# Performance work log

Hardware: AMD Instinct MI355X
Metric: run time of the kernel (lower is better)

The kernel has to match this reference:

```python
import jax, jax.numpy as jnp
import numpy as np

N = 100000
E = 6400000
DIMS = [34, 16, 16, 16, 4]


def setup_inputs() -> dict:
    key = jax.random.key(0)
    ks = jax.random.split(key, 12)
    x = jax.random.normal(ks[0], (N, DIMS[0]), dtype=jnp.float32)
    edge_index = jax.random.randint(ks[1], (2, E), 0, N, dtype=jnp.int64)
    inp = {"x": x, "edge_index": edge_index}
    for i in range(4):
        fan_in, fan_out = DIMS[i], DIMS[i + 1]
        s = (6.0 / (fan_in + fan_out)) ** 0.5  # glorot
        inp[f"W{i+1}"] = jax.random.uniform(ks[2 + 2 * i], (fan_in, fan_out), minval=-s, maxval=s, dtype=jnp.float32)
        inp[f"b{i+1}"] = jnp.zeros((fan_out,), dtype=jnp.float32)
    return inp


def gcn_layer(x, W, b, src, dst, norm):
    # x: [N, din] -> [N, dout]; PyG GCNConv: h = XW, aggregate norm*h[src] into dst, + bias
    h = x @ W
    msgs = h[src] * norm[:, None]                      # [E+N, dout]
    out = jax.ops.segment_sum(msgs, dst, num_segments=N)
    return out + b


def reference(x, edge_index, W1, b1, W2, b2, W3, b3, W4, b4):
    loop = jnp.arange(N, dtype=edge_index.dtype)
    src = jnp.concatenate([edge_index[0], loop])       # add self-loops
    dst = jnp.concatenate([edge_index[1], loop])
    deg = jax.ops.segment_sum(jnp.ones_like(dst, dtype=x.dtype), dst, num_segments=N)
    dinv = jnp.where(deg > 0, jax.lax.rsqrt(deg), 0.0)
    norm = dinv[src] * dinv[dst]                       # symmetric normalization per edge
    h = gcn_layer(x, W1, b1, src, dst, norm)
    h = jax.nn.relu(h)
    h = gcn_layer(h, W2, b2, src, dst, norm)
    h = jax.nn.relu(h)
    h = gcn_layer(h, W3, b3, src, dst, norm)
    h = jax.nn.relu(h)
    return gcn_layer(h, W4, b4, src, dst, norm)
```

## Files before the change

kernel.cpp:

```cpp
#include <hip/hip_runtime.h>
#include <hip/hip_bf16.h>


static constexpr int THREADS   = 256;
static constexpr int BSHIFT    = 7;
static constexpr int NPB       = 128;
static constexpr int MAXB      = 1024;
static constexpr int NCHUNK    = 128;
static constexpr int EPT       = 8;
static constexpr int SSHIFT    = 15;
static constexpr int NSHARD    = 4;
static constexpr int STAGE_CAP = 10240;


__global__ __launch_bounds__(THREADS)
void k_hist(const int* __restrict__ dst, int* __restrict__ hist_part,
            int e, int nbkt, int chunk) {
    __shared__ int h[MAXB];
    for (int t = threadIdx.x; t < nbkt; t += THREADS) h[t] = 0;
    __syncthreads();
    int beg = blockIdx.x * chunk;
    int end = min(e, beg + chunk);
    for (int base = beg; base < end; base += THREADS * EPT) {
        int i = base + (int)threadIdx.x * EPT;
        if (i + EPT <= end) {
            int4 d0 = *(const int4*)(dst + i);
            int4 d1 = *(const int4*)(dst + i + 4);
            atomicAdd(&h[d0.x >> BSHIFT], 1);
            atomicAdd(&h[d0.y >> BSHIFT], 1);
            atomicAdd(&h[d0.z >> BSHIFT], 1);
            atomicAdd(&h[d0.w >> BSHIFT], 1);
            atomicAdd(&h[d1.x >> BSHIFT], 1);
            atomicAdd(&h[d1.y >> BSHIFT], 1);
            atomicAdd(&h[d1.z >> BSHIFT], 1);
            atomicAdd(&h[d1.w >> BSHIFT], 1);
        } else {
            for (int k = i; k < end; k++) atomicAdd(&h[dst[k] >> BSHIFT], 1);
        }
    }
    __syncthreads();
    for (int t = threadIdx.x; t < nbkt; t += THREADS)
        hist_part[(size_t)blockIdx.x * nbkt + t] = h[t];
}

__global__ __launch_bounds__(NCHUNK)
void k_colscan(int* __restrict__ hist_part, int* __restrict__ btot, int nbkt) {
    __shared__ int s[NCHUNK];
    int b = blockIdx.x;
    int v = hist_part[(size_t)threadIdx.x * nbkt + b];
    s[threadIdx.x] = v;
    __syncthreads();
    for (int ofs = 1; ofs < NCHUNK; ofs <<= 1) {
        int t = (threadIdx.x >= ofs) ? s[threadIdx.x - ofs] : 0;
        __syncthreads();
        s[threadIdx.x] += t;
        __syncthreads();
    }
    hist_part[(size_t)threadIdx.x * nbkt + b] = s[threadIdx.x] - v;
    if (threadIdx.x == NCHUNK - 1) btot[b] = s[NCHUNK - 1];
}

__global__ __launch_bounds__(1024)
void k_scan_b(const int* __restrict__ btot, int* __restrict__ bbase,
              int nbkt, int e) {
    __shared__ int s[1024];
    int v = (threadIdx.x < nbkt) ? btot[threadIdx.x] : 0;
    s[threadIdx.x] = v;
    __syncthreads();
    for (int ofs = 1; ofs < 1024; ofs <<= 1) {
        int t = (threadIdx.x >= ofs) ? s[threadIdx.x - ofs] : 0;
        __syncthreads();
        s[threadIdx.x] += t;
        __syncthreads();
    }
    if (threadIdx.x < nbkt) bbase[threadIdx.x] = s[threadIdx.x] - v;
    if (threadIdx.x == 0) bbase[nbkt] = e;
}

__global__ __launch_bounds__(THREADS)
void k_scatter_bkt(const int* __restrict__ src, const int* __restrict__ dst,
                   const int* __restrict__ offs_part, const int* __restrict__ bbase,
                   int* __restrict__ gpack, int e, int nbkt, int chunk) {
    __shared__ int curs[MAXB];
    for (int t = threadIdx.x; t < nbkt; t += THREADS)
        curs[t] = bbase[t] + offs_part[(size_t)blockIdx.x * nbkt + t];
    __syncthreads();
    int beg = blockIdx.x * chunk;
    int end = min(e, beg + chunk);
    for (int base = beg; base < end; base += THREADS * EPT) {
        int i = base + (int)threadIdx.x * EPT;
        if (i + EPT <= end) {
            int4 s0 = *(const int4*)(src + i);
            int4 s1 = *(const int4*)(src + i + 4);
            int4 d0 = *(const int4*)(dst + i);
            int4 d1 = *(const int4*)(dst + i + 4);
            int p0 = atomicAdd(&curs[d0.x >> BSHIFT], 1);
            int p1 = atomicAdd(&curs[d0.y >> BSHIFT], 1);
            int p2 = atomicAdd(&curs[d0.z >> BSHIFT], 1);
            int p3 = atomicAdd(&curs[d0.w >> BSHIFT], 1);
            int p4 = atomicAdd(&curs[d1.x >> BSHIFT], 1);
            int p5 = atomicAdd(&curs[d1.y >> BSHIFT], 1);
            int p6 = atomicAdd(&curs[d1.z >> BSHIFT], 1);
            int p7 = atomicAdd(&curs[d1.w >> BSHIFT], 1);
            gpack[p0] = (s0.x << BSHIFT) | (d0.x & (NPB - 1));
            gpack[p1] = (s0.y << BSHIFT) | (d0.y & (NPB - 1));
            gpack[p2] = (s0.z << BSHIFT) | (d0.z & (NPB - 1));
            gpack[p3] = (s0.w << BSHIFT) | (d0.w & (NPB - 1));
            gpack[p4] = (s1.x << BSHIFT) | (d1.x & (NPB - 1));
            gpack[p5] = (s1.y << BSHIFT) | (d1.y & (NPB - 1));
            gpack[p6] = (s1.z << BSHIFT) | (d1.z & (NPB - 1));
            gpack[p7] = (s1.w << BSHIFT) | (d1.w & (NPB - 1));
        } else {
            for (int k = i; k < end; k++) {
                int d = dst[k];
                int p = atomicAdd(&curs[d >> BSHIFT], 1);
                gpack[p] = (src[k] << BSHIFT) | (d & (NPB - 1));
            }
        }
    }
}

__global__ __launch_bounds__(THREADS)
void k_rowptr2(const int* __restrict__ gpack, const int* __restrict__ bbase,
               int* __restrict__ rowptr2, float* __restrict__ dinv,
               int n, int nbkt) {
    __shared__ int hist2[NPB * NSHARD];
    __shared__ int scn[THREADS];
    int b = blockIdx.x;
    int node0 = b << BSHIFT;
    int nnodes = min(NPB, n - node0);
    int ebeg = bbase[b];
    int eend = bbase[b + 1];
    int tid = threadIdx.x;

    for (int t = tid; t < NPB * NSHARD; t += THREADS) hist2[t] = 0;
    __syncthreads();
    for (int i = ebeg + tid; i < eend; i += THREADS) {
        int g = gpack[i];
        int key = (g & (NPB - 1)) * NSHARD + ((g >> BSHIFT) >> SSHIFT);
        atomicAdd(&hist2[key], 1);
    }
    __syncthreads();
    int v0 = 0, v1 = 0, v2 = 0, v3 = 0, tsum = 0;
    if (tid < NPB) {
        v0 = hist2[tid * NSHARD + 0];
        v1 = hist2[tid * NSHARD + 1];
        v2 = hist2[tid * NSHARD + 2];
        v3 = hist2[tid * NSHARD + 3];
        tsum = v0 + v1 + v2 + v3;
    }
    scn[tid] = tsum;
    __syncthreads();
    for (int ofs = 1; ofs < THREADS; ofs <<= 1) {
        int t = (tid >= ofs) ? scn[tid - ofs] : 0;
        __syncthreads();
        scn[tid] += t;
        __syncthreads();
    }
    int excl = scn[tid] - tsum;
    if (tid < nnodes) {
        int nd = node0 + tid;
        rowptr2[(size_t)nd * NSHARD + 0] = ebeg + excl;
        rowptr2[(size_t)nd * NSHARD + 1] = ebeg + excl + v0;
        rowptr2[(size_t)nd * NSHARD + 2] = ebeg + excl + v0 + v1;
        rowptr2[(size_t)nd * NSHARD + 3] = ebeg + excl + v0 + v1 + v2;
        dinv[nd] = 1.0f / sqrtf((float)(tsum + 1));
    }
    if (b == nbkt - 1 && tid == 0) rowptr2[(size_t)n * NSHARD] = eend;
}

__global__ __launch_bounds__(THREADS)
void k_fill_staged(const int* __restrict__ gpack, const int* __restrict__ bbase,
                   const int* __restrict__ rowptr2, int* __restrict__ csr,
                   int n, int nbkt) {
    __shared__ int curs[NPB * NSHARD];
    __shared__ int staged[STAGE_CAP];
    int b = blockIdx.x;
    int node0 = b << BSHIFT;
    int tid = threadIdx.x;
    int ebeg = bbase[b];
    int eend = bbase[b + 1];
    int len = eend - ebeg;

    for (int t = tid; t < NPB * NSHARD; t += THREADS) {
        int nd = node0 + (t >> 2);
        curs[t] = (nd < n) ? rowptr2[(size_t)nd * NSHARD + (t & 3)] : 0;
    }
    __syncthreads();

    if (len <= STAGE_CAP) {
        for (int i = ebeg + tid; i < eend; i += THREADS) {
            int g = gpack[i];
            int key = (g & (NPB - 1)) * NSHARD + ((g >> BSHIFT) >> SSHIFT);
            int pos = atomicAdd(&curs[key], 1);
            staged[pos - ebeg] = g >> BSHIFT;
        }
        __syncthreads();
        for (int i = tid; i < len; i += THREADS)
            csr[ebeg + i] = staged[i];
    } else {
        for (int i = ebeg + tid; i < eend; i += THREADS) {
            int g = gpack[i];
            int key = (g & (NPB - 1)) * NSHARD + ((g >> BSHIFT) >> SSHIFT);
            int pos = atomicAdd(&curs[key], 1);
            csr[pos] = g >> BSHIFT;
        }
    }
}


__global__ __launch_bounds__(THREADS)
void k_layer_in(const float* __restrict__ x, const float* __restrict__ W,
                const float* __restrict__ dinv, float* __restrict__ hp, int n) {
    __shared__ float sW[34 * 16];
    for (int t = threadIdx.x; t < 34 * 16; t += THREADS) sW[t] = W[t];
    __syncthreads();
    int i = blockIdx.x * THREADS + threadIdx.x;
    if (i >= n) return;
    float di = dinv[i];
    float acc[16];
    #pragma unroll
    for (int j = 0; j < 16; j++) acc[j] = 0.0f;
    const float* xi = x + (size_t)i * 34;
    #pragma unroll
    for (int k = 0; k < 34; k++) {
        float xk = xi[k];
        #pragma unroll
        for (int j = 0; j < 16; j++) acc[j] = fmaf(xk, sW[k * 16 + j], acc[j]);
    }
    float4* o = (float4*)(hp + (size_t)i * 16);
    o[0] = make_float4(acc[0] * di, acc[1] * di, acc[2] * di, acc[3] * di);
    o[1] = make_float4(acc[4] * di, acc[5] * di, acc[6] * di, acc[7] * di);
    o[2] = make_float4(acc[8] * di, acc[9] * di, acc[10] * di, acc[11] * di);
    o[3] = make_float4(acc[12] * di, acc[13] * di, acc[14] * di, acc[15] * di);
}

__global__ __launch_bounds__(THREADS)
void k_layer_mid2(const float* __restrict__ part, const float* __restrict__ W,
                  const float* __restrict__ bprev, const float* __restrict__ dinv,
                  float* __restrict__ hp, int n) {
    __shared__ float sW[16 * 16];
    __shared__ float sB[16];
    for (int t = threadIdx.x; t < 16 * 16; t += THREADS) sW[t] = W[t];
    if (threadIdx.x < 16) sB[threadIdx.x] = bprev[threadIdx.x];
    __syncthreads();
    int i = blockIdx.x * THREADS + threadIdx.x;
    if (i >= n) return;
    float di = dinv[i];
    size_t stride = (size_t)n * 4;
    const float4* p = (const float4*)(part + (size_t)i * 16);
    float4 a0 = p[0], a1 = p[1], a2 = p[2], a3 = p[3];
    #pragma unroll
    for (int s = 1; s < NSHARD; s++) {
        float4 q0 = p[s * stride + 0], q1 = p[s * stride + 1];
        float4 q2 = p[s * stride + 2], q3 = p[s * stride + 3];
        a0.x += q0.x; a0.y += q0.y; a0.z += q0.z; a0.w += q0.w;
        a1.x += q1.x; a1.y += q1.y; a1.z += q1.z; a1.w += q1.w;
        a2.x += q2.x; a2.y += q2.y; a2.z += q2.z; a2.w += q2.w;
        a3.x += q3.x; a3.y += q3.y; a3.z += q3.z; a3.w += q3.w;
    }
    float xin[16] = {a0.x, a0.y, a0.z, a0.w, a1.x, a1.y, a1.z, a1.w,
                     a2.x, a2.y, a2.z, a2.w, a3.x, a3.y, a3.z, a3.w};
    #pragma unroll
    for (int k = 0; k < 16; k++)
        xin[k] = fmaxf(fmaf(di, xin[k], sB[k]), 0.0f);
    float acc[16];
    #pragma unroll
    for (int j = 0; j < 16; j++) acc[j] = 0.0f;
    #pragma unroll
    for (int k = 0; k < 16; k++) {
        float xk = xin[k];
        #pragma unroll
        for (int j = 0; j < 16; j++) acc[j] = fmaf(xk, sW[k * 16 + j], acc[j]);
    }
    float4* o = (float4*)(hp + (size_t)i * 16);
    o[0] = make_float4(acc[0] * di, acc[1] * di, acc[2] * di, acc[3] * di);
    o[1] = make_float4(acc[4] * di, acc[5] * di, acc[6] * di, acc[7] * di);
    o[2] = make_float4(acc[8] * di, acc[9] * di, acc[10] * di, acc[11] * di);
    o[3] = make_float4(acc[12] * di, acc[13] * di, acc[14] * di, acc[15] * di);
}

__global__ __launch_bounds__(THREADS)
void k_layer_last2(const float* __restrict__ part, const float* __restrict__ W,
                   const float* __restrict__ bprev, const float* __restrict__ dinv,
                   float* __restrict__ hp4, int n) {
    __shared__ float sW[16 * 4];
    __shared__ float sB[16];
    for (int t = threadIdx.x; t < 16 * 4; t += THREADS) sW[t] = W[t];
    if (threadIdx.x < 16) sB[threadIdx.x] = bprev[threadIdx.x];
    __syncthreads();
    int i = blockIdx.x * THREADS + threadIdx.x;
    if (i >= n) return;
    float di = dinv[i];
    size_t stride = (size_t)n * 4;
    const float4* p = (const float4*)(part + (size_t)i * 16);
    float4 a0 = p[0], a1 = p[1], a2 = p[2], a3 = p[3];
    #pragma unroll
    for (int s = 1; s < NSHARD; s++) {
        float4 q0 = p[s * stride + 0], q1 = p[s * stride + 1];
        float4 q2 = p[s * stride + 2], q3 = p[s * stride + 3];
        a0.x += q0.x; a0.y += q0.y; a0.z += q0.z; a0.w += q0.w;
        a1.x += q1.x; a1.y += q1.y; a1.z += q1.z; a1.w += q1.w;
        a2.x += q2.x; a2.y += q2.y; a2.z += q2.z; a2.w += q2.w;
        a3.x += q3.x; a3.y += q3.y; a3.z += q3.z; a3.w += q3.w;
    }
    float xin[16] = {a0.x, a0.y, a0.z, a0.w, a1.x, a1.y, a1.z, a1.w,
                     a2.x, a2.y, a2.z, a2.w, a3.x, a3.y, a3.z, a3.w};
    #pragma unroll
    for (int k = 0; k < 16; k++)
        xin[k] = fmaxf(fmaf(di, xin[k], sB[k]), 0.0f);
    float acc[4];
    #pragma unroll
    for (int j = 0; j < 4; j++) acc[j] = 0.0f;
    #pragma unroll
    for (int k = 0; k < 16; k++) {
        float xk = xin[k];
        #pragma unroll
        for (int j = 0; j < 4; j++) acc[j] = fmaf(xk, sW[k * 4 + j], acc[j]);
    }
    *(float4*)(hp4 + (size_t)i * 4) =
        make_float4(acc[0] * di, acc[1] * di, acc[2] * di, acc[3] * di);
}


__global__ __launch_bounds__(THREADS, 8)
void k_gather16s(const int* __restrict__ rowptr2, const int* __restrict__ csr,
                 const float* __restrict__ hp, float* __restrict__ part, int n) {
    int shard = blockIdx.x & (NSHARD - 1);
    int rg    = blockIdx.x >> 2;
    int row   = rg * 16 + ((int)threadIdx.x >> 4);
    int lane  = threadIdx.x & 15;
    if (row >= n) return;
    int base = (threadIdx.x & 63) & ~15;

    int beg = rowptr2[(size_t)row * NSHARD + shard];
    int end = rowptr2[(size_t)row * NSHARD + shard + 1];
    int len = end - beg;

    float a0 = ((row >> SSHIFT) == shard) ? hp[(size_t)row * 16 + lane] : 0.0f;
    float a1 = 0.f, a2 = 0.f, a3 = 0.f;

    int s0 = 0, s1 = 0;
    if (len > 0)  s0 = csr[min(beg + lane, end - 1)];
    if (len > 16) s1 = csr[min(beg + 16 + lane, end - 1)];

    {
        int cnt = len;
        #pragma unroll
        for (int k = 0; k < 16; k += 4) {
            int sk0 = __shfl(s0, base + k + 0, 64);
            int sk1 = __shfl(s0, base + k + 1, 64);
            int sk2 = __shfl(s0, base + k + 2, 64);
            int sk3 = __shfl(s0, base + k + 3, 64);
            float v0 = hp[(size_t)sk0 * 16 + lane];
            float v1 = hp[(size_t)sk1 * 16 + lane];
            float v2 = hp[(size_t)sk2 * 16 + lane];
            float v3 = hp[(size_t)sk3 * 16 + lane];
            a0 += (k + 0 < cnt) ? v0 : 0.0f;
            a1 += (k + 1 < cnt) ? v1 : 0.0f;
            a2 += (k + 2 < cnt) ? v2 : 0.0f;
            a3 += (k + 3 < cnt) ? v3 : 0.0f;
        }
    }
    {
        int cnt = len - 16;
        #pragma unroll
        for (int k = 0; k < 16; k += 4) {
            int sk0 = __shfl(s1, base + k + 0, 64);
            int sk1 = __shfl(s1, base + k + 1, 64);
            int sk2 = __shfl(s1, base + k + 2, 64);
            int sk3 = __shfl(s1, base + k + 3, 64);
            float v0 = hp[(size_t)sk0 * 16 + lane];
            float v1 = hp[(size_t)sk1 * 16 + lane];
            float v2 = hp[(size_t)sk2 * 16 + lane];
            float v3 = hp[(size_t)sk3 * 16 + lane];
            a0 += (k + 0 < cnt) ? v0 : 0.0f;
            a1 += (k + 1 < cnt) ? v1 : 0.0f;
            a2 += (k + 2 < cnt) ? v2 : 0.0f;
            a3 += (k + 3 < cnt) ? v3 : 0.0f;
        }
    }
    for (int e = beg + 32; e < end; e += 16) {
        int s = csr[min(e + lane, end - 1)];
        int cnt = end - e;
        #pragma unroll
        for (int k = 0; k < 16; k += 4) {
            int sk0 = __shfl(s, base + k + 0, 64);
            int sk1 = __shfl(s, base + k + 1, 64);
            int sk2 = __shfl(s, base + k + 2, 64);
            int sk3 = __shfl(s, base + k + 3, 64);
            float v0 = hp[(size_t)sk0 * 16 + lane];
            float v1 = hp[(size_t)sk1 * 16 + lane];
            float v2 = hp[(size_t)sk2 * 16 + lane];
            float v3 = hp[(size_t)sk3 * 16 + lane];
            a0 += (k + 0 < cnt) ? v0 : 0.0f;
            a1 += (k + 1 < cnt) ? v1 : 0.0f;
            a2 += (k + 2 < cnt) ? v2 : 0.0f;
            a3 += (k + 3 < cnt) ? v3 : 0.0f;
        }
    }
    part[((size_t)shard * n + row) * 16 + lane] = (a0 + a1) + (a2 + a3);
}

__global__ __launch_bounds__(THREADS, 8)
void k_gather4_final(const int* __restrict__ rowptr2, const int* __restrict__ csr,
                     const float* __restrict__ hp, float* __restrict__ outp,
                     const float* __restrict__ dinv, const float* __restrict__ bias,
                     int n) {
    int tid = blockIdx.x * THREADS + threadIdx.x;
    int row = tid >> 4;
    int sub = threadIdx.x & 15;
    int e4  = sub >> 2;
    int ch  = sub & 3;
    if (row >= n) return;
    int base = (threadIdx.x & 63) & ~15;

    int beg = rowptr2[(size_t)row * NSHARD];
    int end = rowptr2[(size_t)(row + 1) * NSHARD];
    int len = end - beg;

    float a = (e4 == 0) ? hp[(size_t)row * 4 + ch] : 0.0f;

    int s0 = 0, s1 = 0;
    if (len > 0)  s0 = csr[min(beg + sub, end - 1)];
    if (len > 16) s1 = csr[min(beg + 16 + sub, end - 1)];

    {
        int cnt = len;
        #pragma unroll
        for (int k = 0; k < 4; k++) {
            int idx = k * 4 + e4;
            int sk = __shfl(s0, base + idx, 64);
            float v = hp[(size_t)sk * 4 + ch];
            a += (idx < cnt) ? v : 0.0f;
        }
    }
    {
        int cnt = len - 16;
        #pragma unroll
        for (int k = 0; k < 4; k++) {
            int idx = k * 4 + e4;
            int sk = __shfl(s1, base + idx, 64);
            float v = hp[(size_t)sk * 4 + ch];
            a += (idx < cnt) ? v : 0.0f;
        }
    }
    for (int e = beg + 32; e < end; e += 16) {
        int s = csr[min(e + sub, end - 1)];
        int cnt = end - e;
        #pragma unroll
        for (int k = 0; k < 4; k++) {
            int idx = k * 4 + e4;
            int sk = __shfl(s, base + idx, 64);
            float v = hp[(size_t)sk * 4 + ch];
            a += (idx < cnt) ? v : 0.0f;
        }
    }
    a += __shfl_xor(a, 4, 64);
    a += __shfl_xor(a, 8, 64);
    if (e4 == 0) outp[(size_t)row * 4 + ch] = fmaf(dinv[row], a, bias[ch]);
}


__global__ __launch_bounds__(THREADS)
void k_zero(int* __restrict__ p, int n) {
    int i = blockIdx.x * THREADS + threadIdx.x;
    if (i < n) p[i] = 0;
}

__global__ __launch_bounds__(THREADS)
void k_count_deg(const int* __restrict__ dst, int* __restrict__ deg, int e) {
    int i = blockIdx.x * THREADS + threadIdx.x;
    if (i >= e) return;
    atomicAdd(&deg[dst[i]], 1);
}

__global__ __launch_bounds__(THREADS)
void k_dinv(const int* __restrict__ deg, float* __restrict__ dinv, int n) {
    int i = blockIdx.x * THREADS + threadIdx.x;
    if (i < n) dinv[i] = 1.0f / sqrtf((float)(deg[i] + 1));
}

__global__ __launch_bounds__(THREADS)
void k_scan1(const int* __restrict__ deg, int* __restrict__ rowptr,
             int* __restrict__ bsum, int n) {
    __shared__ int s[THREADS];
    int i = blockIdx.x * THREADS + threadIdx.x;
    int v = (i < n) ? deg[i] : 0;
    s[threadIdx.x] = v;
    __syncthreads();
    for (int ofs = 1; ofs < THREADS; ofs <<= 1) {
        int t = (threadIdx.x >= ofs) ? s[threadIdx.x - ofs] : 0;
        __syncthreads();
        s[threadIdx.x] += t;
        __syncthreads();
    }
    if (i < n) rowptr[i] = s[threadIdx.x] - v;
    if (threadIdx.x == THREADS - 1) bsum[blockIdx.x] = s[THREADS - 1];
}

__global__ __launch_bounds__(1024)
void k_scan2(int* __restrict__ bsum, int nb) {
    __shared__ int s[1024];
    int v = (threadIdx.x < nb) ? bsum[threadIdx.x] : 0;
    s[threadIdx.x] = v;
    __syncthreads();
    for (int ofs = 1; ofs < 1024; ofs <<= 1) {
        int t = (threadIdx.x >= ofs) ? s[threadIdx.x - ofs] : 0;
        __syncthreads();
        s[threadIdx.x] += t;
        __syncthreads();
    }
    if (threadIdx.x < nb) bsum[threadIdx.x] = s[threadIdx.x] - v;
}

__global__ __launch_bounds__(THREADS)
void k_scan3(int* __restrict__ rowptr, const int* __restrict__ bsum,
             int* __restrict__ cursor, int n, int e) {
    int i = blockIdx.x * THREADS + threadIdx.x;
    if (i < n) {
        int r = rowptr[i] + bsum[blockIdx.x];
        rowptr[i] = r;
        cursor[i] = r;
    }
    if (i == 0) rowptr[n] = e;
}

__global__ __launch_bounds__(THREADS)
void k_fill_cursor(const int* __restrict__ src, const int* __restrict__ dst,
                   int* __restrict__ cursor, int* __restrict__ csr, int e) {
    int i = blockIdx.x * THREADS + threadIdx.x;
    if (i >= e) return;
    int pos = atomicAdd(&cursor[dst[i]], 1);
    csr[pos] = src[i];
}

template<int DIN, int DOUT, bool TRANSFORM>
__global__ __launch_bounds__(THREADS)
void k_layer(const float* __restrict__ in, const float* __restrict__ W,
             const float* __restrict__ bprev, const float* __restrict__ dinv,
             float* __restrict__ hp, int n) {
    __shared__ float sW[DIN * DOUT];
    for (int t = threadIdx.x; t < DIN * DOUT; t += THREADS) sW[t] = W[t];
    __syncthreads();
    int i = blockIdx.x * THREADS + threadIdx.x;
    if (i >= n) return;
    float di = dinv[i];
    float xin[DIN];
    #pragma unroll
    for (int k = 0; k < DIN; k++) xin[k] = in[(size_t)i * DIN + k];
    if constexpr (TRANSFORM) {
        #pragma unroll
        for (int k = 0; k < DIN; k++)
            xin[k] = fmaxf(fmaf(di, xin[k], bprev[k]), 0.0f);
    }
    float acc[DOUT];
    #pragma unroll
    for (int j = 0; j < DOUT; j++) acc[j] = 0.0f;
    #pragma unroll
    for (int k = 0; k < DIN; k++) {
        float xk = xin[k];
        #pragma unroll
        for (int j = 0; j < DOUT; j++) acc[j] = fmaf(xk, sW[k * DOUT + j], acc[j]);
    }
    #pragma unroll
    for (int j = 0; j < DOUT; j++) hp[(size_t)i * DOUT + j] = acc[j] * di;
}

template<int D, bool FINAL>
__global__ __launch_bounds__(THREADS)
void k_gather(const int* __restrict__ rowptr, const int* __restrict__ csr,
              const float* __restrict__ hp, float* __restrict__ outp,
              const float* __restrict__ dinv, const float* __restrict__ bias,
              int n) {
    int tid  = blockIdx.x * THREADS + threadIdx.x;
    int row  = tid / D;
    int lane = tid & (D - 1);
    if (row >= n) return;
    int base = (threadIdx.x & 63) & ~(D - 1);
    int beg = rowptr[row];
    int end = rowptr[row + 1];
    float a0 = hp[(size_t)row * D + lane];
    float a1 = 0.f, a2 = 0.f, a3 = 0.f;
    int e = beg;
    for (; e + D <= end; e += D) {
        int s = csr[e + lane];
        #pragma unroll
        for (int k = 0; k < D; k += 4) {
            int s0 = __shfl(s, base + k + 0, 64);
            int s1 = __shfl(s, base + k + 1, 64);
            int s2 = __shfl(s, base + k + 2, 64);
            int s3 = __shfl(s, base + k + 3, 64);
            a0 += hp[(size_t)s0 * D + lane];
            a1 += hp[(size_t)s1 * D + lane];
            a2 += hp[(size_t)s2 * D + lane];
            a3 += hp[(size_t)s3 * D + lane];
        }
    }
    if (e < end) {
        int idx = e + lane;
        int s = (idx < end) ? csr[idx] : 0;
        int cnt = end - e;
        for (int k = 0; k < cnt; k++) {
            int sk = __shfl(s, base + k, 64);
            a0 += hp[(size_t)sk * D + lane];
        }
    }
    float acc = (a0 + a1) + (a2 + a3);
    if constexpr (FINAL) {
        outp[(size_t)row * D + lane] = fmaf(dinv[row], acc, bias[lane]);
    } else {
        outp[(size_t)row * D + lane] = acc;
    }
}


extern "C" void kernel_launch(void* const* d_in, const int* in_sizes, int n_in,
                              void* d_out, int out_size, void* d_ws, size_t ws_size,
                              hipStream_t stream) {
    const float* x   = (const float*)d_in[0];
    const int*   ei  = (const int*)d_in[1];
    const float* W1  = (const float*)d_in[2];
    const float* b1  = (const float*)d_in[3];
    const float* W2  = (const float*)d_in[4];
    const float* b2  = (const float*)d_in[5];
    const float* W3  = (const float*)d_in[6];
    const float* b3  = (const float*)d_in[7];
    const float* W4  = (const float*)d_in[8];
    const float* b4  = (const float*)d_in[9];
    float*       out = (float*)d_out;

    const int N = in_sizes[0] / 34;
    const int E = in_sizes[1] / 2;
    const int* src = ei;
    const int* dst = ei + E;

    const int gN  = (N + THREADS - 1) / THREADS;

    const int nbkt  = (N + NPB - 1) >> BSHIFT;
    const int chunk = (((E + NCHUNK - 1) / NCHUNK) + EPT - 1) & ~(EPT - 1);
    const int gG    = ((N + 15) / 16) * NSHARD;
    const int gF    = (int)(((size_t)N * 16 + THREADS - 1) / THREADS);

    {
        char* ws = (char*)d_ws;
        size_t off = 0;
        auto alloc = [&](size_t bytes) -> void* {
            void* p = ws + off;
            off += (bytes + 255) & ~(size_t)255;
            return p;
        };
        float* dinv    = (float*)alloc((size_t)N * 4);
        float* hp      = (float*)alloc((size_t)N * 16 * 4);
        float* part    = (float*)alloc((size_t)NSHARD * N * 16 * 4);
        float* hp4     = (float*)alloc((size_t)N * 4 * 4);
        int*   rowptr2 = (int*)  alloc(((size_t)N * NSHARD + 1) * 4);
        int*   csr     = (int*)  alloc((size_t)E * 4);
        int*   gpack   = (int*)  alloc((size_t)E * 4);
        int*   offsp   = (int*)  alloc((size_t)NCHUNK * nbkt * 4);
        int*   btot    = (int*)  alloc((size_t)nbkt * 4);
        int*   bbase   = (int*)  alloc((size_t)(nbkt + 1) * 4);

        bool aligned16 = (((uintptr_t)src & 15) == 0) && (((uintptr_t)dst & 15) == 0);
        bool fast_ok = (nbkt <= MAXB) && (off <= ws_size) && aligned16 &&
                       (N <= (1 << (31 - BSHIFT - 1))) &&
                       (N <= (NSHARD << SSHIFT));

        if (fast_ok) {
            k_hist        <<<NCHUNK, THREADS, 0, stream>>>(dst, offsp, E, nbkt, chunk);
            k_colscan     <<<nbkt, NCHUNK, 0, stream>>>(offsp, btot, nbkt);
            k_scan_b      <<<1, 1024, 0, stream>>>(btot, bbase, nbkt, E);
            k_scatter_bkt <<<NCHUNK, THREADS, 0, stream>>>(src, dst, offsp, bbase,
                                                           gpack, E, nbkt, chunk);
            k_rowptr2     <<<nbkt, THREADS, 0, stream>>>(gpack, bbase, rowptr2,
                                                         dinv, N, nbkt);
            k_fill_staged <<<nbkt, THREADS, 0, stream>>>(gpack, bbase, rowptr2,
                                                         csr, N, nbkt);

            k_layer_in <<<gN, THREADS, 0, stream>>>(x, W1, dinv, hp, N);
            k_gather16s<<<gG, THREADS, 0, stream>>>(rowptr2, csr, hp, part, N);

            k_layer_mid2<<<gN, THREADS, 0, stream>>>(part, W2, b1, dinv, hp, N);
            k_gather16s<<<gG, THREADS, 0, stream>>>(rowptr2, csr, hp, part, N);

            k_layer_mid2<<<gN, THREADS, 0, stream>>>(part, W3, b2, dinv, hp, N);
            k_gather16s<<<gG, THREADS, 0, stream>>>(rowptr2, csr, hp, part, N);

            k_layer_last2<<<gN, THREADS, 0, stream>>>(part, W4, b3, dinv, hp4, N);
            k_gather4_final<<<gF, THREADS, 0, stream>>>(rowptr2, csr, hp4, out,
                                                        dinv, b4, N);
            return;
        }
    }

    {
        char* ws = (char*)d_ws;
        size_t off = 0;
        auto alloc = [&](size_t bytes) -> void* {
            void* p = ws + off;
            off += (bytes + 255) & ~(size_t)255;
            return p;
        };
        int*   deg    = (int*)  alloc((size_t)N * 4);
        float* dinv   = (float*)alloc((size_t)N * 4);
        float* bufA   = (float*)alloc((size_t)N * 16 * 4);
        float* bufB   = (float*)alloc((size_t)N * 16 * 4);
        int*   rowptr = (int*)  alloc((size_t)(N + 1) * 4);
        int*   cursor = (int*)  alloc((size_t)N * 4);
        const int nb  = (N + THREADS - 1) / THREADS;
        int*   bsum   = (int*)  alloc((size_t)nb * 4);
        int*   csr    = (int*)  alloc((size_t)E * 4);

        const int gE  = (E + THREADS - 1) / THREADS;
        const int g16 = (int)(((size_t)N * 16 + THREADS - 1) / THREADS);
        const int g4  = (int)(((size_t)N * 4 + THREADS - 1) / THREADS);

        k_zero<<<gN, THREADS, 0, stream>>>(deg, N);
        k_count_deg<<<gE, THREADS, 0, stream>>>(dst, deg, E);
        k_dinv<<<gN, THREADS, 0, stream>>>(deg, dinv, N);
        k_scan1<<<nb, THREADS, 0, stream>>>(deg, rowptr, bsum, N);
        k_scan2<<<1, 1024, 0, stream>>>(bsum, nb);
        k_scan3<<<nb, THREADS, 0, stream>>>(rowptr, bsum, cursor, N, E);
        k_fill_cursor<<<gE, THREADS, 0, stream>>>(src, dst, cursor, csr, E);

        k_layer<34, 16, false><<<gN, THREADS, 0, stream>>>(x, W1, nullptr, dinv, bufA, N);
        k_gather<16, false><<<g16, THREADS, 0, stream>>>(rowptr, csr, bufA, bufB, nullptr, nullptr, N);

        k_layer<16, 16, true><<<gN, THREADS, 0, stream>>>(bufB, W2, b1, dinv, bufA, N);
        k_gather<16, false><<<g16, THREADS, 0, stream>>>(rowptr, csr, bufA, bufB, nullptr, nullptr, N);

        k_layer<16, 16, true><<<gN, THREADS, 0, stream>>>(bufB, W3, b2, dinv, bufA, N);
        k_gather<16, false><<<g16, THREADS, 0, stream>>>(rowptr, csr, bufA, bufB, nullptr, nullptr, N);

        k_layer<16, 4, true><<<gN, THREADS, 0, stream>>>(bufB, W4, b3, dinv, bufA, N);
        k_gather<4, true><<<g4, THREADS, 0, stream>>>(rowptr, csr, bufA, out, dinv, b4, N);
    }
}
```

Baseline: 315.0 us.

## Sort edge chunks locally in LDS before writing bucket runs to global

The bucket scatter now splits edges into many smaller fixed-size chunks (about 481 blocks instead of 128). Each block first counting-sorts its chunk into shared memory by destination bucket, then copies each bucket's run contiguously to global memory. This replaces random 4-byte global stores with mostly coalesced run writes and raises parallelism. The cost is a larger per-block LDS footprint (about 61KB), which limits occupancy, plus a bigger partial histogram and a wider column scan.

```diff
diff --git a/kernel.cpp b/kernel.cpp
--- a/kernel.cpp
+++ b/kernel.cpp
@@ -6,7 +6,8 @@
 static constexpr int BSHIFT    = 7;
 static constexpr int NPB       = 128;
 static constexpr int MAXB      = 1024;
-static constexpr int NCHUNK    = 128;
+static constexpr int CH        = 13312;
+static constexpr int MAXCHB    = 512;
 static constexpr int EPT       = 8;
 static constexpr int SSHIFT    = 15;
 static constexpr int NSHARD    = 4;
@@ -15,12 +16,12 @@
 
 __global__ __launch_bounds__(THREADS)
 void k_hist(const int* __restrict__ dst, int* __restrict__ hist_part,
-            int e, int nbkt, int chunk) {
+            int e, int nbkt) {
     __shared__ int h[MAXB];
     for (int t = threadIdx.x; t < nbkt; t += THREADS) h[t] = 0;
     __syncthreads();
-    int beg = blockIdx.x * chunk;
-    int end = min(e, beg + chunk);
+    int beg = blockIdx.x * CH;
+    int end = min(e, beg + CH);
     for (int base = beg; base < end; base += THREADS * EPT) {
         int i = base + (int)threadIdx.x * EPT;
         if (i + EPT <= end) {
@@ -43,21 +44,23 @@
         hist_part[(size_t)blockIdx.x * nbkt + t] = h[t];
 }
 
-__global__ __launch_bounds__(NCHUNK)
-void k_colscan(int* __restrict__ hist_part, int* __restrict__ btot, int nbkt) {
-    __shared__ int s[NCHUNK];
+__global__ __launch_bounds__(MAXCHB)
+void k_colscan(const int* __restrict__ hist_part, int* __restrict__ offs,
+               int* __restrict__ btot, int nbkt, int nblk) {
+    __shared__ int s[MAXCHB];
     int b = blockIdx.x;
-    int v = hist_part[(size_t)threadIdx.x * nbkt + b];
+    int v = (threadIdx.x < nblk) ? hist_part[(size_t)threadIdx.x * nbkt + b] : 0;
     s[threadIdx.x] = v;
     __syncthreads();
-    for (int ofs = 1; ofs < NCHUNK; ofs <<= 1) {
+    for (int ofs = 1; ofs < MAXCHB; ofs <<= 1) {
         int t = (threadIdx.x >= ofs) ? s[threadIdx.x - ofs] : 0;
         __syncthreads();
         s[threadIdx.x] += t;
         __syncthreads();
     }
-    hist_part[(size_t)threadIdx.x * nbkt + b] = s[threadIdx.x] - v;
-    if (threadIdx.x == NCHUNK - 1) btot[b] = s[NCHUNK - 1];
+    if (threadIdx.x < nblk)
+        offs[(size_t)threadIdx.x * nbkt + b] = s[threadIdx.x] - v;
+    if (threadIdx.x == MAXCHB - 1) btot[b] = s[MAXCHB - 1];
 }
 
 __global__ __launch_bounds__(1024)
@@ -78,17 +81,48 @@
 }
 
 __global__ __launch_bounds__(THREADS)
-void k_scatter_bkt(const int* __restrict__ src, const int* __restrict__ dst,
-                   const int* __restrict__ offs_part, const int* __restrict__ bbase,
-                   int* __restrict__ gpack, int e, int nbkt, int chunk) {
+void k_sortchunk(const int* __restrict__ src, const int* __restrict__ dst,
+                 const int* __restrict__ hist_part, const int* __restrict__ offs,
+                 const int* __restrict__ bbase, int* __restrict__ gpack,
+                 int e, int nbkt) {
+    __shared__ int hist[MAXB];
     __shared__ int curs[MAXB];
-    for (int t = threadIdx.x; t < nbkt; t += THREADS)
-        curs[t] = bbase[t] + offs_part[(size_t)blockIdx.x * nbkt + t];
-    __syncthreads();
-    int beg = blockIdx.x * chunk;
-    int end = min(e, beg + chunk);
+    __shared__ int scn[THREADS];
+    __shared__ int staged[CH];
+    int tid = threadIdx.x;
+    int blk = blockIdx.x;
+
+    for (int t = tid; t < nbkt; t += THREADS) hist[t] = hist_part[(size_t)blk * nbkt + t];
+    __syncthreads();
+
+    int base_t = tid * 4;
+    int v0 = (base_t + 0 < nbkt) ? hist[base_t + 0] : 0;
+    int v1 = (base_t + 1 < nbkt) ? hist[base_t + 1] : 0;
+    int v2 = (base_t + 2 < nbkt) ? hist[base_t + 2] : 0;
+    int v3 = (base_t + 3 < nbkt) ? hist[base_t + 3] : 0;
+    int tsum = v0 + v1 + v2 + v3;
+    scn[tid] = tsum;
+    __syncthreads();
+    for (int ofs = 1; ofs < THREADS; ofs <<= 1) {
+        int t = (tid >= ofs) ? scn[tid - ofs] : 0;
+        __syncthreads();
+        scn[tid] += t;
+        __syncthreads();
+    }
+    int run = scn[tid] - tsum;
+    if (base_t + 0 < nbkt) curs[base_t + 0] = run;
+    run += v0;
+    if (base_t + 1 < nbkt) curs[base_t + 1] = run;
+    run += v1;
+    if (base_t + 2 < nbkt) curs[base_t + 2] = run;
+    run += v2;
+    if (base_t + 3 < nbkt) curs[base_t + 3] = run;
+    __syncthreads();
+
+    int beg = blk * CH;
+    int end = min(e, beg + CH);
     for (int base = beg; base < end; base += THREADS * EPT) {
-        int i = base + (int)threadIdx.x * EPT;
+        int i = base + tid * EPT;
         if (i + EPT <= end) {
             int4 s0 = *(const int4*)(src + i);
             int4 s1 = *(const int4*)(src + i + 4);
@@ -102,21 +136,32 @@
             int p5 = atomicAdd(&curs[d1.y >> BSHIFT], 1);
             int p6 = atomicAdd(&curs[d1.z >> BSHIFT], 1);
             int p7 = atomicAdd(&curs[d1.w >> BSHIFT], 1);
-            gpack[p0] = (s0.x << BSHIFT) | (d0.x & (NPB - 1));
-            gpack[p1] = (s0.y << BSHIFT) | (d0.y & (NPB - 1));
-            gpack[p2] = (s0.z << BSHIFT) | (d0.z & (NPB - 1));
-            gpack[p3] = (s0.w << BSHIFT) | (d0.w & (NPB - 1));
-            gpack[p4] = (s1.x << BSHIFT) | (d1.x & (NPB - 1));
-            gpack[p5] = (s1.y << BSHIFT) | (d1.y & (NPB - 1));
-            gpack[p6] = (s1.z << BSHIFT) | (d1.z & (NPB - 1));
-            gpack[p7] = (s1.w << BSHIFT) | (d1.w & (NPB - 1));
+            staged[p0] = (s0.x << BSHIFT) | (d0.x & (NPB - 1));
+            staged[p1] = (s0.y << BSHIFT) | (d0.y & (NPB - 1));
+            staged[p2] = (s0.z << BSHIFT) | (d0.z & (NPB - 1));
+            staged[p3] = (s0.w << BSHIFT) | (d0.w & (NPB - 1));
+            staged[p4] = (s1.x << BSHIFT) | (d1.x & (NPB - 1));
+            staged[p5] = (s1.y << BSHIFT) | (d1.y & (NPB - 1));
+            staged[p6] = (s1.z << BSHIFT) | (d1.z & (NPB - 1));
+            staged[p7] = (s1.w << BSHIFT) | (d1.w & (NPB - 1));
         } else {
             for (int k = i; k < end; k++) {
                 int d = dst[k];
                 int p = atomicAdd(&curs[d >> BSHIFT], 1);
-                gpack[p] = (src[k] << BSHIFT) | (d & (NPB - 1));
+                staged[p] = (src[k] << BSHIFT) | (d & (NPB - 1));
             }
         }
+    }
+    __syncthreads();
+
+    int wid = tid >> 6, lane = tid & 63;
+    for (int b = wid; b < nbkt; b += 4) {
+        int len = hist[b];
+        if (len == 0) continue;
+        int loc = curs[b] - len;
+        int gb  = bbase[b] + offs[(size_t)blk * nbkt + b];
+        for (int k = lane; k < len; k += 64)
+            gpack[gb + k] = staged[loc + k];
     }
 }
 
@@ -635,10 +680,10 @@
     const int* src = ei;
     const int* dst = ei + E;
 
-    const int gN  = (N + THREADS - 1) / THREADS;
+    const int gN = (N + THREADS - 1) / THREADS;
 
     const int nbkt  = (N + NPB - 1) >> BSHIFT;
-    const int chunk = (((E + NCHUNK - 1) / NCHUNK) + EPT - 1) & ~(EPT - 1);
+    const int nblkS = (E + CH - 1) / CH;
     const int gG    = ((N + 15) / 16) * NSHARD;
     const int gF    = (int)(((size_t)N * 16 + THREADS - 1) / THREADS);
 
@@ -657,21 +702,23 @@
         int*   rowptr2 = (int*)  alloc(((size_t)N * NSHARD + 1) * 4);
         int*   csr     = (int*)  alloc((size_t)E * 4);
         int*   gpack   = (int*)  alloc((size_t)E * 4);
-        int*   offsp   = (int*)  alloc((size_t)NCHUNK * nbkt * 4);
+        int*   histp   = (int*)  alloc((size_t)nblkS * nbkt * 4);
+        int*   offs2   = (int*)  alloc((size_t)nblkS * nbkt * 4);
         int*   btot    = (int*)  alloc((size_t)nbkt * 4);
         int*   bbase   = (int*)  alloc((size_t)(nbkt + 1) * 4);
 
         bool aligned16 = (((uintptr_t)src & 15) == 0) && (((uintptr_t)dst & 15) == 0);
-        bool fast_ok = (nbkt <= MAXB) && (off <= ws_size) && aligned16 &&
+        bool fast_ok = (nbkt <= MAXB) && (nblkS <= MAXCHB) && (off <= ws_size) &&
+                       aligned16 &&
                        (N <= (1 << (31 - BSHIFT - 1))) &&
                        (N <= (NSHARD << SSHIFT));
 
         if (fast_ok) {
-            k_hist        <<<NCHUNK, THREADS, 0, stream>>>(dst, offsp, E, nbkt, chunk);
-            k_colscan     <<<nbkt, NCHUNK, 0, stream>>>(offsp, btot, nbkt);
+            k_hist        <<<nblkS, THREADS, 0, stream>>>(dst, histp, E, nbkt);
+            k_colscan     <<<nbkt, MAXCHB, 0, stream>>>(histp, offs2, btot, nbkt, nblkS);
             k_scan_b      <<<1, 1024, 0, stream>>>(btot, bbase, nbkt, E);
-            k_scatter_bkt <<<NCHUNK, THREADS, 0, stream>>>(src, dst, offsp, bbase,
-                                                           gpack, E, nbkt, chunk);
+            k_sortchunk   <<<nblkS, THREADS, 0, stream>>>(src, dst, histp, offs2,
+                                                          bbase, gpack, E, nbkt);
             k_rowptr2     <<<nbkt, THREADS, 0, stream>>>(gpack, bbase, rowptr2,
                                                          dinv, N, nbkt);
             k_fill_staged <<<nbkt, THREADS, 0, stream>>>(gpack, bbase, rowptr2,
```

Result: slower. 328.4 us (+4.2%).
